# Optimization experiments

Measured on AMD Instinct MI355X. Metric: run time of the kernel, lower is better.

The kernel has to match this reference:

```python
import jax, jax.numpy as jnp
import numpy as np
from jax import lax

N = 100000      # number of nodes (== ninput)
E = 3200000     # number of edges per adjacency
NHID = 128
EPS = 1e-12     # torch F.normalize eps


def spmm(src, dst, w, x):
    # sparse adj @ x : out[i] = sum_{e: dst[e]==i} w[e] * x[src[e]]
    return jax.ops.segment_sum(w[:, None] * x[src], dst, num_segments=N)


def l2norm(x):
    # F.normalize(x, p=2, dim=1)
    n = jnp.sqrt(jnp.sum(x * x, axis=1, keepdims=True))
    return x / jnp.maximum(n, EPS)


def mlp(x, L1, bl1, L2, bl2, L3, bl3):
    # dropout == 0.0 -> identity; chunking is a memory optimization, same math
    h = jax.nn.relu(x @ L1 + bl1)
    h = jax.nn.relu(h @ L2 + bl2)
    return h @ L3 + bl3  # [N, 1]


def setup_inputs() -> dict:
    key = jax.random.key(0)
    ks = jax.random.split(key, 32)
    d = {}
    d["adj1_src"] = jax.random.randint(ks[0], (E,), 0, N, dtype=jnp.int32)
    d["adj1_dst"] = jax.random.randint(ks[1], (E,), 0, N, dtype=jnp.int32)
    d["adj1_w"] = jax.random.uniform(ks[2], (E,), dtype=jnp.float32)
    d["adj2_src"] = jax.random.randint(ks[3], (E,), 0, N, dtype=jnp.int32)
    d["adj2_dst"] = jax.random.randint(ks[4], (E,), 0, N, dtype=jnp.int32)
    d["adj2_w"] = jax.random.uniform(ks[5], (E,), dtype=jnp.float32)
    d["W1"] = jax.random.normal(ks[6], (N, NHID), dtype=jnp.float32) * 0.05
    d["b1"] = jnp.zeros((NHID,), jnp.float32)
    for i, k in zip(range(2, 7), ks[7:12]):
        d[f"W{i}"] = jax.random.normal(k, (NHID, NHID), dtype=jnp.float32) * (1.0 / np.sqrt(NHID))
        d[f"b{i}"] = jnp.zeros((NHID,), jnp.float32)
    d["L1"] = jax.random.normal(ks[12], (NHID, 2 * NHID), dtype=jnp.float32) * (1.0 / np.sqrt(NHID))
    d["bl1"] = jnp.zeros((2 * NHID,), jnp.float32)
    d["L2"] = jax.random.normal(ks[13], (2 * NHID, 2 * NHID), dtype=jnp.float32) * (1.0 / np.sqrt(2 * NHID))
    d["bl2"] = jnp.zeros((2 * NHID,), jnp.float32)
    d["L3"] = jax.random.normal(ks[14], (2 * NHID, 1), dtype=jnp.float32) * (1.0 / np.sqrt(2 * NHID))
    d["bl3"] = jnp.zeros((1,), jnp.float32)
    return d


def reference(adj1_src, adj1_dst, adj1_w, adj2_src, adj2_dst, adj2_w,
              W1, b1, W2, b2, W3, b3, W4, b4, W5, b5, W6, b6,
              L1, bl1, L2, bl2, L3, bl3):
    def branch(src, dst, w):
        x1 = l2norm(jax.nn.relu(spmm(src, dst, w, W1) + b1))
        x2 = l2norm(jax.nn.relu(spmm(src, dst, w, x1 @ W2) + b2))
        x3 = l2norm(jax.nn.relu(spmm(src, dst, w, x2 @ W3) + b3))
        x4 = l2norm(jax.nn.relu(spmm(src, dst, w, x3 @ W4) + b4))
        x5 = l2norm(jax.nn.relu(spmm(src, dst, w, x4 @ W5) + b5))
        x6 = jax.nn.relu(spmm(src, dst, w, x5 @ W6) + b6)
        x7 = lax.stop_gradient(x1 + x2 + x3 + x4 + x5 + x6)  # .detach()
        s = jnp.zeros((N, 1), jnp.float32)
        for xi in (x1, x2, x3, x4, x5):  # computed under torch.no_grad()
            s = s + lax.stop_gradient(mlp(xi, L1, bl1, L2, bl2, L3, bl3))
        s = s + mlp(x6, L1, bl1, L2, bl2, L3, bl3)
        s = s + mlp(x7, L1, bl1, L2, bl2, L3, bl3)
        return s / 7.0

    score1 = branch(adj1_src, adj1_dst, adj1_w)
    score2 = branch(adj2_src, adj2_dst, adj2_w)
    return score1 * score2
```

## Files before the change

### kernel.cpp

```cpp
#include <hip/hip_runtime.h>

#define NN 100000
#define NE 3200000
#define HID 128
#define NNH ((size_t)NN * HID)

typedef __attribute__((ext_vector_type(8))) _Float16 f16x8;
typedef __attribute__((ext_vector_type(4))) _Float16 f16x4;
typedef __attribute__((ext_vector_type(4))) float f32x4;

#define SWZ(row, k) ((k) ^ (((row) & 7) << 3))

__global__ void zero_k(int* p, int n) {
    int i = blockIdx.x * 256 + threadIdx.x;
    if (i < n) p[i] = 0;
}

__global__ void hist_k(const int* __restrict__ dst, int* __restrict__ cnt) {
    int e = blockIdx.x * 256 + threadIdx.x;
    if (e < NE) atomicAdd(&cnt[dst[e]], 1);
}

__global__ __launch_bounds__(1024) void scanA_k(int* __restrict__ rowptr, int* __restrict__ bsum, int n) {
    __shared__ int wsum[16];
    int tid = threadIdx.x;
    int lane = tid & 63, wid = tid >> 6;
    int idx = blockIdx.x * 1024 + tid;
    int v = (idx < n) ? rowptr[idx] : 0;
    int s = v;
#pragma unroll
    for (int o = 1; o < 64; o <<= 1) {
        int t = __shfl_up(s, o, 64);
        if (lane >= o) s += t;
    }
    if (lane == 63) wsum[wid] = s;
    __syncthreads();
    if (wid == 0) {
        int ws = (lane < 16) ? wsum[lane] : 0;
#pragma unroll
        for (int o = 1; o < 16; o <<= 1) {
            int t = __shfl_up(ws, o, 64);
            if (lane >= o) ws += t;
        }
        if (lane < 16) wsum[lane] = ws;
    }
    __syncthreads();
    int woff = (wid == 0) ? 0 : wsum[wid - 1];
    if (idx < n) rowptr[idx] = woff + s - v;
    if (tid == 0) bsum[blockIdx.x] = wsum[15];
}

__global__ void scanB_k(int* __restrict__ bsum, int* __restrict__ rowptr, int nb, int n) {
    if (threadIdx.x == 0) {
        int run = 0;
        for (int i = 0; i < nb; ++i) {
            int t = bsum[i];
            bsum[i] = run;
            run += t;
        }
        rowptr[n] = run;
    }
}

__global__ void scanC_k(int* __restrict__ rowptr, int* __restrict__ cursor,
                        const int* __restrict__ bsum, int n) {
    int idx = blockIdx.x * 256 + threadIdx.x;
    if (idx < n) {
        int v = rowptr[idx] + bsum[idx >> 10];
        rowptr[idx] = v;
        cursor[idx] = v;
    }
}

__global__ void scatter_k(const int* __restrict__ src, const int* __restrict__ dst,
                          const float* __restrict__ w, int* __restrict__ cursor,
                          unsigned* __restrict__ ep) {
    int e = blockIdx.x * 256 + threadIdx.x;
    if (e < NE) {
        int d = dst[e];
        int pos = atomicAdd(&cursor[d], 1);
        ushort hb = __builtin_bit_cast(ushort, (_Float16)w[e]);
        ep[pos] = ((unsigned)src[e] << 15) | (unsigned)hb;
    }
}

template <bool DESC>
__device__ inline unsigned bsort64(unsigned v, int lane) {
#pragma unroll
    for (int k = 2; k <= 64; k <<= 1)
#pragma unroll
        for (int j = k >> 1; j > 0; j >>= 1) {
            unsigned o = __shfl_xor(v, j, 64);
            bool keepmin = ((((lane & j) == 0) == ((lane & k) == 0))) ^ DESC;
            unsigned mn = v < o ? v : o, mx = v < o ? o : v;
            v = keepmin ? mn : mx;
        }
    return v;
}

__device__ inline unsigned bmerge64(unsigned v, int lane) {
#pragma unroll
    for (int j = 32; j > 0; j >>= 1) {
        unsigned o = __shfl_xor(v, j, 64);
        unsigned mn = v < o ? v : o, mx = v < o ? o : v;
        v = ((lane & j) == 0) ? mn : mx;
    }
    return v;
}

__global__ void sort_k(const int* __restrict__ rowptr, unsigned* __restrict__ ep) {
    int row = blockIdx.x * 4 + (threadIdx.x >> 6);
    int lane = threadIdx.x & 63;
    if (row >= NN) return;
    int e0 = rowptr[row], e1 = rowptr[row + 1];
    int deg = e1 - e0;
    if (deg <= 1) return;
    if (deg <= 64) {
        unsigned v = (e0 + lane < e1) ? ep[e0 + lane] : 0xFFFFFFFFu;
        v = bsort64<false>(v, lane);
        if (e0 + lane < e1) ep[e0 + lane] = v;
    } else if (deg <= 128) {
        unsigned a = (e0 + lane < e1) ? ep[e0 + lane] : 0xFFFFFFFFu;
        unsigned b = (e0 + 64 + lane < e1) ? ep[e0 + 64 + lane] : 0xFFFFFFFFu;
        a = bsort64<false>(a, lane);
        b = bsort64<true>(b, lane);
        unsigned mn = a < b ? a : b, mx = a < b ? b : a;
        a = bmerge64(mn, lane);
        b = bmerge64(mx, lane);
        if (e0 + lane < e1) ep[e0 + lane] = a;
        if (e0 + 64 + lane < e1) ep[e0 + 64 + lane] = b;
    }
}

__global__ void convT_k(const float* __restrict__ W, _Float16* __restrict__ WT, int K, int N) {
    int idx = blockIdx.x * 256 + threadIdx.x;
    if (idx < K * N) {
        int k = idx / N, n = idx % N;
        WT[n * K + k] = (_Float16)W[idx];
    }
}

__global__ void conv4_k(const float* __restrict__ A, _Float16* __restrict__ B, int n4) {
    int i = blockIdx.x * 256 + threadIdx.x;
    if (i < n4) {
        float4 v = ((const float4*)A)[i];
        f16x4 h;
        h.x = (_Float16)v.x; h.y = (_Float16)v.y; h.z = (_Float16)v.z; h.w = (_Float16)v.w;
        ((f16x4*)B)[i] = h;
    }
}

template <bool EPI>
__global__ void spmm_k(const _Float16* __restrict__ x, const int* __restrict__ rowptr,
                       const unsigned* __restrict__ ep, const float* __restrict__ bias,
                       _Float16* __restrict__ outx) {
    int row = blockIdx.x * 4 + (threadIdx.x >> 6);
    int l = threadIdx.x & 63;
    int q = l >> 4, li = l & 15;
    if (row >= NN) return;
    int e0 = rowptr[row], e1 = rowptr[row + 1];
    float acc[8] = {};
#pragma unroll 4
    for (int e = e0 + q; e < e1; e += 4) {
        unsigned r = ep[e];
        int s = r >> 15;
        float w = (float)__builtin_bit_cast(_Float16, (ushort)(r & 0x7FFFu));
        f16x8 v = *(const f16x8*)(x + (size_t)s * HID + li * 8);
#pragma unroll
        for (int j = 0; j < 8; ++j) acc[j] += w * (float)v[j];
    }
#pragma unroll
    for (int j = 0; j < 8; ++j) {
        acc[j] += __shfl_xor(acc[j], 16, 64);
        acc[j] += __shfl_xor(acc[j], 32, 64);
    }
    if (EPI) {
        const float4* bp = (const float4*)(bias + li * 8);
        float4 b0 = bp[0], b1 = bp[1];
        acc[0] = fmaxf(acc[0] + b0.x, 0.f); acc[1] = fmaxf(acc[1] + b0.y, 0.f);
        acc[2] = fmaxf(acc[2] + b0.z, 0.f); acc[3] = fmaxf(acc[3] + b0.w, 0.f);
        acc[4] = fmaxf(acc[4] + b1.x, 0.f); acc[5] = fmaxf(acc[5] + b1.y, 0.f);
        acc[6] = fmaxf(acc[6] + b1.z, 0.f); acc[7] = fmaxf(acc[7] + b1.w, 0.f);
        float ss = 0.f;
#pragma unroll
        for (int j = 0; j < 8; ++j) ss += acc[j] * acc[j];
        ss += __shfl_xor(ss, 1, 64);
        ss += __shfl_xor(ss, 2, 64);
        ss += __shfl_xor(ss, 4, 64);
        ss += __shfl_xor(ss, 8, 64);
        float sc = 1.0f / fmaxf(sqrtf(ss), 1e-12f);
#pragma unroll
        for (int j = 0; j < 8; ++j) acc[j] *= sc;
    }
    if (q == 0) {
        f16x8 ho;
#pragma unroll
        for (int j = 0; j < 8; ++j) ho[j] = (_Float16)acc[j];
        *(f16x8*)(outx + (size_t)row * HID + li * 8) = ho;
    }
}

template <bool NORM>
__global__ __launch_bounds__(256) void trans_mlp_k(
    const _Float16* __restrict__ Y,
    const _Float16* __restrict__ WT,
    const float* __restrict__ bw,
    _Float16* __restrict__ Xo,
    const _Float16* __restrict__ L1T, const float* __restrict__ bl1,
    const _Float16* __restrict__ L2T, const float* __restrict__ bl2,
    const float* __restrict__ L3, const float* __restrict__ bl3,
    float* __restrict__ sacc) {
    __shared__ _Float16 Xs[64][128];
    __shared__ _Float16 H1s[64][256];
    __shared__ float red[4][64];
    int t = threadIdx.x;
    int w = t >> 6, l = t & 63;
    int g = l >> 4, li = l & 15;
    int rowBase = blockIdx.x * 64;

#pragma unroll
    for (int i = 0; i < 4; ++i) {
        int idx = t + i * 256;
        int r = idx >> 4, c8 = idx & 15;
        int gr = rowBase + r;
        f16x8 v = (gr < NN) ? *(const f16x8*)(Y + (size_t)gr * 128 + c8 * 8)
                            : (f16x8)(_Float16)0.f;
        *(f16x8*)&Xs[r][SWZ(r, c8 * 8)] = v;
    }
    __syncthreads();

    int cW = w * 32;
    f32x4 accw[4][2] = {};
#pragma unroll
    for (int ks = 0; ks < 4; ++ks) {
        int kb = ks * 32 + g * 8;
        f16x8 a[4];
#pragma unroll
        for (int mt = 0; mt < 4; ++mt) {
            int r = mt * 16 + li;
            a[mt] = *(const f16x8*)&Xs[r][SWZ(r, kb)];
        }
#pragma unroll
        for (int nt = 0; nt < 2; ++nt) {
            f16x8 b = *(const f16x8*)(WT + (size_t)(cW + nt * 16 + li) * 128 + kb);
#pragma unroll
            for (int mt = 0; mt < 4; ++mt)
                accw[mt][nt] = __builtin_amdgcn_mfma_f32_16x16x32_f16(a[mt], b, accw[mt][nt], 0, 0, 0);
        }
    }
    float vv[4][2][4];
    float b0 = bw[cW + li], b1v = bw[cW + 16 + li];
#pragma unroll
    for (int mt = 0; mt < 4; ++mt)
#pragma unroll
        for (int r4 = 0; r4 < 4; ++r4) {
            vv[mt][0][r4] = fmaxf(accw[mt][0][r4] + b0, 0.f);
            vv[mt][1][r4] = fmaxf(accw[mt][1][r4] + b1v, 0.f);
        }
    if (NORM) {
#pragma unroll
        for (int mt = 0; mt < 4; ++mt)
#pragma unroll
            for (int r4 = 0; r4 < 4; ++r4) {
                float ps = vv[mt][0][r4] * vv[mt][0][r4] + vv[mt][1][r4] * vv[mt][1][r4];
                ps += __shfl_xor(ps, 1, 64);
                ps += __shfl_xor(ps, 2, 64);
                ps += __shfl_xor(ps, 4, 64);
                ps += __shfl_xor(ps, 8, 64);
                if (li == 0) red[w][mt * 16 + g * 4 + r4] = ps;
            }
        __syncthreads();
        if (t < 64) {
            float s = red[0][t] + red[1][t] + red[2][t] + red[3][t];
            red[0][t] = 1.f / fmaxf(sqrtf(s), 1e-12f);
        }
        __syncthreads();
    } else {
        __syncthreads();
    }
#pragma unroll
    for (int mt = 0; mt < 4; ++mt)
#pragma unroll
        for (int r4 = 0; r4 < 4; ++r4) {
            int row = mt * 16 + g * 4 + r4;
            float sc = NORM ? red[0][row] : 1.f;
            _Float16 h0 = (_Float16)(vv[mt][0][r4] * sc);
            _Float16 h1 = (_Float16)(vv[mt][1][r4] * sc);
            Xs[row][SWZ(row, cW + li)] = h0;
            Xs[row][SWZ(row, cW + 16 + li)] = h1;
            int gr = rowBase + row;
            if (gr < NN) {
                Xo[(size_t)gr * 128 + cW + li] = h0;
                Xo[(size_t)gr * 128 + cW + 16 + li] = h1;
            }
        }
    __syncthreads();

    int cM = w * 64;
    f32x4 acc[4][4] = {};
#pragma unroll
    for (int ks = 0; ks < 4; ++ks) {
        int kb = ks * 32 + g * 8;
        f16x8 a[4];
#pragma unroll
        for (int mt = 0; mt < 4; ++mt) {
            int r = mt * 16 + li;
            a[mt] = *(const f16x8*)&Xs[r][SWZ(r, kb)];
        }
#pragma unroll
        for (int nt = 0; nt < 4; ++nt) {
            int n = cM + nt * 16 + li;
            f16x8 b = *(const f16x8*)(L1T + (size_t)n * 128 + kb);
#pragma unroll
            for (int mt = 0; mt < 4; ++mt)
                acc[mt][nt] = __builtin_amdgcn_mfma_f32_16x16x32_f16(a[mt], b, acc[mt][nt], 0, 0, 0);
        }
    }
#pragma unroll
    for (int nt = 0; nt < 4; ++nt) {
        int col = cM + nt * 16 + li;
        float bb = bl1[col];
#pragma unroll
        for (int mt = 0; mt < 4; ++mt)
#pragma unroll
            for (int r4 = 0; r4 < 4; ++r4) {
                int row = mt * 16 + g * 4 + r4;
                H1s[row][SWZ(row, col)] = (_Float16)fmaxf(acc[mt][nt][r4] + bb, 0.f);
            }
    }
    __syncthreads();

    f32x4 acc2[4][4] = {};
#pragma unroll
    for (int ks = 0; ks < 8; ++ks) {
        int kb = ks * 32 + g * 8;
        f16x8 a[4];
#pragma unroll
        for (int mt = 0; mt < 4; ++mt) {
            int r = mt * 16 + li;
            a[mt] = *(const f16x8*)&H1s[r][SWZ(r, kb)];
        }
#pragma unroll
        for (int nt = 0; nt < 4; ++nt) {
            int n = cM + nt * 16 + li;
            f16x8 b = *(const f16x8*)(L2T + (size_t)n * 256 + kb);
#pragma unroll
            for (int mt = 0; mt < 4; ++mt)
                acc2[mt][nt] = __builtin_amdgcn_mfma_f32_16x16x32_f16(a[mt], b, acc2[mt][nt], 0, 0, 0);
        }
    }
    float part[4][4] = {};
#pragma unroll
    for (int nt = 0; nt < 4; ++nt) {
        int col = cM + nt * 16 + li;
        float bb = bl2[col];
        float l3v = L3[col];
#pragma unroll
        for (int mt = 0; mt < 4; ++mt)
#pragma unroll
            for (int r4 = 0; r4 < 4; ++r4)
                part[mt][r4] += fmaxf(acc2[mt][nt][r4] + bb, 0.f) * l3v;
    }
#pragma unroll
    for (int mt = 0; mt < 4; ++mt)
#pragma unroll
        for (int r4 = 0; r4 < 4; ++r4) {
            float p = part[mt][r4];
            p += __shfl_xor(p, 1, 64);
            p += __shfl_xor(p, 2, 64);
            p += __shfl_xor(p, 4, 64);
            p += __shfl_xor(p, 8, 64);
            if (li == 0) red[w][mt * 16 + g * 4 + r4] = p;
        }
    __syncthreads();
    if (t < 64) {
        int gr = rowBase + t;
        if (gr < NN)
            sacc[gr] += red[0][t] + red[1][t] + red[2][t] + red[3][t] + bl3[0];
    }
}

template <bool SUM6, bool INIT>
__global__ __launch_bounds__(256) void mlp_fused_k(
    const _Float16* __restrict__ X,
    const _Float16* __restrict__ L1T, const float* __restrict__ bl1,
    const _Float16* __restrict__ L2T, const float* __restrict__ bl2,
    const float* __restrict__ L3, const float* __restrict__ bl3,
    float* __restrict__ sacc) {
    __shared__ _Float16 Xs[64][128];
    __shared__ _Float16 H1s[64][256];
    __shared__ float red[4][64];
    int t = threadIdx.x;
    int w = t >> 6, l = t & 63;
    int g = l >> 4, li = l & 15;
    int rowBase = blockIdx.x * 64;

#pragma unroll
    for (int i = 0; i < 4; ++i) {
        int idx = t + i * 256;
        int r = idx >> 4, c8 = idx & 15;
        int gr = rowBase + r;
        if (SUM6) {
            float s[8] = {};
            if (gr < NN) {
#pragma unroll
                for (int l6 = 0; l6 < 6; ++l6) {
                    f16x8 v = *(const f16x8*)(X + (size_t)l6 * NNH + (size_t)gr * HID + c8 * 8);
#pragma unroll
                    for (int j = 0; j < 8; ++j) s[j] += (float)v[j];
                }
            }
            f16x8 hv;
#pragma unroll
            for (int j = 0; j < 8; ++j) hv[j] = (_Float16)s[j];
            *(f16x8*)&Xs[r][SWZ(r, c8 * 8)] = hv;
        } else {
            f16x8 v = (gr < NN) ? *(const f16x8*)(X + (size_t)gr * HID + c8 * 8)
                                : (f16x8)(_Float16)0.f;
            *(f16x8*)&Xs[r][SWZ(r, c8 * 8)] = v;
        }
    }
    __syncthreads();

    int cM = w * 64;
    f32x4 acc[4][4] = {};
#pragma unroll
    for (int ks = 0; ks < 4; ++ks) {
        int kb = ks * 32 + g * 8;
        f16x8 a[4];
#pragma unroll
        for (int mt = 0; mt < 4; ++mt) {
            int r = mt * 16 + li;
            a[mt] = *(const f16x8*)&Xs[r][SWZ(r, kb)];
        }
#pragma unroll
        for (int nt = 0; nt < 4; ++nt) {
            int n = cM + nt * 16 + li;
            f16x8 b = *(const f16x8*)(L1T + (size_t)n * 128 + kb);
#pragma unroll
            for (int mt = 0; mt < 4; ++mt)
                acc[mt][nt] = __builtin_amdgcn_mfma_f32_16x16x32_f16(a[mt], b, acc[mt][nt], 0, 0, 0);
        }
    }
#pragma unroll
    for (int nt = 0; nt < 4; ++nt) {
        int col = cM + nt * 16 + li;
        float bb = bl1[col];
#pragma unroll
        for (int mt = 0; mt < 4; ++mt)
#pragma unroll
            for (int r4 = 0; r4 < 4; ++r4) {
                int row = mt * 16 + g * 4 + r4;
                H1s[row][SWZ(row, col)] = (_Float16)fmaxf(acc[mt][nt][r4] + bb, 0.f);
            }
    }
    __syncthreads();

    f32x4 acc2[4][4] = {};
#pragma unroll
    for (int ks = 0; ks < 8; ++ks) {
        int kb = ks * 32 + g * 8;
        f16x8 a[4];
#pragma unroll
        for (int mt = 0; mt < 4; ++mt) {
            int r = mt * 16 + li;
            a[mt] = *(const f16x8*)&H1s[r][SWZ(r, kb)];
        }
#pragma unroll
        for (int nt = 0; nt < 4; ++nt) {
            int n = cM + nt * 16 + li;
            f16x8 b = *(const f16x8*)(L2T + (size_t)n * 256 + kb);
#pragma unroll
            for (int mt = 0; mt < 4; ++mt)
                acc2[mt][nt] = __builtin_amdgcn_mfma_f32_16x16x32_f16(a[mt], b, acc2[mt][nt], 0, 0, 0);
        }
    }
    float part[4][4] = {};
#pragma unroll
    for (int nt = 0; nt < 4; ++nt) {
        int col = cM + nt * 16 + li;
        float bb = bl2[col];
        float l3v = L3[col];
#pragma unroll
        for (int mt = 0; mt < 4; ++mt)
#pragma unroll
            for (int r4 = 0; r4 < 4; ++r4)
                part[mt][r4] += fmaxf(acc2[mt][nt][r4] + bb, 0.f) * l3v;
    }
#pragma unroll
    for (int mt = 0; mt < 4; ++mt)
#pragma unroll
        for (int r4 = 0; r4 < 4; ++r4) {
            float p = part[mt][r4];
            p += __shfl_xor(p, 1, 64);
            p += __shfl_xor(p, 2, 64);
            p += __shfl_xor(p, 4, 64);
            p += __shfl_xor(p, 8, 64);
            if (li == 0) red[w][mt * 16 + g * 4 + r4] = p;
        }
    __syncthreads();
    if (t < 64) {
        int gr = rowBase + t;
        if (gr < NN) {
            float s = red[0][t] + red[1][t] + red[2][t] + red[3][t] + bl3[0];
            if (INIT) sacc[gr] = s; else sacc[gr] += s;
        }
    }
}

__global__ void score_store_k(const float* __restrict__ sacc, float* __restrict__ dst) {
    int i = blockIdx.x * 256 + threadIdx.x;
    if (i < NN) dst[i] = sacc[i] * (1.f / 7.f);
}

__global__ void final_mul_k(const float* __restrict__ sacc, const float* __restrict__ score1,
                            float* __restrict__ out) {
    int i = blockIdx.x * 256 + threadIdx.x;
    if (i < NN) out[i] = score1[i] * (sacc[i] * (1.f / 7.f));
}

extern "C" void kernel_launch(void* const* d_in, const int* in_sizes, int n_in,
                              void* d_out, int out_size, void* d_ws, size_t ws_size,
                              hipStream_t stream) {
    const int* asrc[2] = {(const int*)d_in[0], (const int*)d_in[3]};
    const int* adst[2] = {(const int*)d_in[1], (const int*)d_in[4]};
    const float* aw[2] = {(const float*)d_in[2], (const float*)d_in[5]};
    const float* W1 = (const float*)d_in[6];
    const float* b1 = (const float*)d_in[7];
    const float* Wk[5] = {(const float*)d_in[8], (const float*)d_in[10], (const float*)d_in[12],
                          (const float*)d_in[14], (const float*)d_in[16]};
    const float* bk[5] = {(const float*)d_in[9], (const float*)d_in[11], (const float*)d_in[13],
                          (const float*)d_in[15], (const float*)d_in[17]};
    const float* L1 = (const float*)d_in[18];
    const float* bl1 = (const float*)d_in[19];
    const float* L2 = (const float*)d_in[20];
    const float* bl2 = (const float*)d_in[21];
    const float* L3 = (const float*)d_in[22];
    const float* bl3 = (const float*)d_in[23];
    float* out = (float*)d_out;

    char* p = (char*)d_ws;
    _Float16* L1T = (_Float16*)p; p += 65536;
    _Float16* L2T = (_Float16*)p; p += 131072;
    _Float16* WkT = (_Float16*)p; p += 163840;
    _Float16* W1h = (_Float16*)p; p += NNH * 2;
    _Float16* tmp = (_Float16*)p; p += NNH * 2;
    _Float16* xbuf = (_Float16*)p; p += 6 * NNH * 2;
    float* sacc = (float*)p; p += (size_t)NN * 4;
    float* score1 = (float*)p; p += (size_t)NN * 4;
    unsigned* ep = (unsigned*)p; p += (size_t)NE * 4;
    int* rowptr = (int*)p; p += (size_t)(NN + 1) * 4;
    int* cursor = (int*)p; p += (size_t)NN * 4;
    int* bsum = (int*)p; p += 512;

    const int GE = (NE + 255) / 256;
    const int GN = (NN + 255) / 256;
    const int GS = (NN + 3) / 4;
    const int GM = (NN + 63) / 64;
    const int NB = (NN + 1023) / 1024;

    convT_k<<<(128 * 256 + 255) / 256, 256, 0, stream>>>(L1, L1T, 128, 256);
    convT_k<<<(256 * 256 + 255) / 256, 256, 0, stream>>>(L2, L2T, 256, 256);
    for (int l = 0; l < 5; ++l)
        convT_k<<<(128 * 128 + 255) / 256, 256, 0, stream>>>(Wk[l], WkT + (size_t)l * 16384, 128, 128);
    conv4_k<<<(NN * HID / 4 + 255) / 256, 256, 0, stream>>>(W1, W1h, NN * HID / 4);

    for (int br = 0; br < 2; ++br) {
        zero_k<<<GN, 256, 0, stream>>>(rowptr, NN + 1);
        hist_k<<<GE, 256, 0, stream>>>(adst[br], rowptr);
        scanA_k<<<NB, 1024, 0, stream>>>(rowptr, bsum, NN);
        scanB_k<<<1, 64, 0, stream>>>(bsum, rowptr, NB, NN);
        scanC_k<<<GN, 256, 0, stream>>>(rowptr, cursor, bsum, NN);
        scatter_k<<<GE, 256, 0, stream>>>(asrc[br], adst[br], aw[br], cursor, ep);
        sort_k<<<GS, 256, 0, stream>>>(rowptr, ep);

        spmm_k<true><<<GS, 256, 0, stream>>>(W1h, rowptr, ep, b1, xbuf);
        mlp_fused_k<false, true><<<GM, 256, 0, stream>>>(xbuf, L1T, bl1, L2T, bl2, L3, bl3, sacc);

        for (int l = 0; l < 5; ++l) {
            spmm_k<false><<<GS, 256, 0, stream>>>(xbuf + (size_t)l * NNH, rowptr, ep, b1, tmp);
            _Float16* xo = xbuf + (size_t)(l + 1) * NNH;
            if (l < 4)
                trans_mlp_k<true><<<GM, 256, 0, stream>>>(tmp, WkT + (size_t)l * 16384, bk[l], xo,
                                                          L1T, bl1, L2T, bl2, L3, bl3, sacc);
            else
                trans_mlp_k<false><<<GM, 256, 0, stream>>>(tmp, WkT + (size_t)l * 16384, bk[l], xo,
                                                           L1T, bl1, L2T, bl2, L3, bl3, sacc);
        }

        mlp_fused_k<true, false><<<GM, 256, 0, stream>>>(xbuf, L1T, bl1, L2T, bl2, L3, bl3, sacc);

        if (br == 0)
            score_store_k<<<GN, 256, 0, stream>>>(sacc, score1);
        else
            final_mul_k<<<GN, 256, 0, stream>>>(sacc, score1, out);
    }
}
```

Measured before the change: 2.842 ms.

## Window SpMM by source-row ranges to improve gather cache locality

Adds a bounds kernel that binary-searches each row's sorted edge list to split it into 8 source-node windows. The SpMM is rewritten so each block owns 33 destination rows in each of two halves and sweeps windows in order, accumulating partial sums in shared memory. All blocks then read the same source-row range at about the same time, which should keep the gathered feature rows cache-resident. The costs are extra per-window bound loads, one wave handling each row-window serially with 2 halves per lane, fewer blocks in flight, and no guarantee that blocks stay in step.

```diff
diff --git a/kernel.cpp b/kernel.cpp
--- a/kernel.cpp
+++ b/kernel.cpp
@@ -4,9 +4,15 @@
 #define NE 3200000
 #define HID 128
 #define NNH ((size_t)NN * HID)
+#define HALF 50000
+#define NWIN 8
+#define WROWS 12500
+#define RPB 33
+#define NBLK 1516
 
 typedef __attribute__((ext_vector_type(8))) _Float16 f16x8;
 typedef __attribute__((ext_vector_type(4))) _Float16 f16x4;
+typedef __attribute__((ext_vector_type(2))) _Float16 f16x2;
 typedef __attribute__((ext_vector_type(4))) float f32x4;
 
 #define SWZ(row, k) ((k) ^ (((row) & 7) << 3))
@@ -132,6 +138,24 @@
     }
 }
 
+__global__ void bounds_k(const int* __restrict__ rowptr, const unsigned* __restrict__ ep,
+                         int* __restrict__ bnd) {
+    int r = blockIdx.x * 256 + threadIdx.x;
+    if (r >= NN) return;
+    int e0 = rowptr[r], e1 = rowptr[r + 1];
+    bnd[r] = e0;
+    bnd[(size_t)NWIN * NN + r] = e1;
+    for (int wdx = 1; wdx < NWIN; ++wdx) {
+        unsigned key = (unsigned)(wdx * WROWS) << 15;
+        int lo = e0, hi = e1;
+        while (lo < hi) {
+            int mid = (lo + hi) >> 1;
+            if (ep[mid] < key) lo = mid + 1; else hi = mid;
+        }
+        bnd[(size_t)wdx * NN + r] = lo;
+    }
+}
+
 __global__ void convT_k(const float* __restrict__ W, _Float16* __restrict__ WT, int K, int N) {
     int idx = blockIdx.x * 256 + threadIdx.x;
     if (idx < K * N) {
@@ -151,61 +175,67 @@
 }
 
 template <bool EPI>
-__global__ void spmm_k(const _Float16* __restrict__ x, const int* __restrict__ rowptr,
-                       const unsigned* __restrict__ ep, const float* __restrict__ bias,
-                       _Float16* __restrict__ outx) {
-    int row = blockIdx.x * 4 + (threadIdx.x >> 6);
-    int l = threadIdx.x & 63;
-    int q = l >> 4, li = l & 15;
-    if (row >= NN) return;
-    int e0 = rowptr[row], e1 = rowptr[row + 1];
-    float acc[8] = {};
+__global__ __launch_bounds__(256) void spmm_win_k(const _Float16* __restrict__ x,
+                                                  const int* __restrict__ bnd,
+                                                  const unsigned* __restrict__ ep,
+                                                  const float* __restrict__ bias,
+                                                  _Float16* __restrict__ outx) {
+    __shared__ float accs[RPB][HID];
+    int tid = threadIdx.x;
+    int w = tid >> 6, lane = tid & 63;
+    for (int g = 0; g < 2; ++g) {
+        int rowBase = g * HALF + blockIdx.x * RPB;
+        int rowLim = (g + 1) * HALF;
+        for (int i = tid; i < RPB * HID; i += 256) ((float*)accs)[i] = 0.f;
+        __syncthreads();
+        for (int win = 0; win < NWIN; ++win) {
+            const int* b0p = bnd + (size_t)win * NN;
+            const int* b1p = bnd + (size_t)(win + 1) * NN;
+            for (int j = w; j < RPB; j += 4) {
+                int r = rowBase + j;
+                if (r >= rowLim) break;
+                int e0 = b0p[r], e1 = b1p[r];
+                if (e0 == e1) continue;
+                float a0 = 0.f, a1 = 0.f;
 #pragma unroll 4
-    for (int e = e0 + q; e < e1; e += 4) {
-        unsigned r = ep[e];
-        int s = r >> 15;
-        float w = (float)__builtin_bit_cast(_Float16, (ushort)(r & 0x7FFFu));
-        f16x8 v = *(const f16x8*)(x + (size_t)s * HID + li * 8);
-#pragma unroll
-        for (int j = 0; j < 8; ++j) acc[j] += w * (float)v[j];
-    }
-#pragma unroll
-    for (int j = 0; j < 8; ++j) {
-        acc[j] += __shfl_xor(acc[j], 16, 64);
-        acc[j] += __shfl_xor(acc[j], 32, 64);
-    }
-    if (EPI) {
-        const float4* bp = (const float4*)(bias + li * 8);
-        float4 b0 = bp[0], b1 = bp[1];
-        acc[0] = fmaxf(acc[0] + b0.x, 0.f); acc[1] = fmaxf(acc[1] + b0.y, 0.f);
-        acc[2] = fmaxf(acc[2] + b0.z, 0.f); acc[3] = fmaxf(acc[3] + b0.w, 0.f);
-        acc[4] = fmaxf(acc[4] + b1.x, 0.f); acc[5] = fmaxf(acc[5] + b1.y, 0.f);
-        acc[6] = fmaxf(acc[6] + b1.z, 0.f); acc[7] = fmaxf(acc[7] + b1.w, 0.f);
-        float ss = 0.f;
-#pragma unroll
-        for (int j = 0; j < 8; ++j) ss += acc[j] * acc[j];
-        ss += __shfl_xor(ss, 1, 64);
-        ss += __shfl_xor(ss, 2, 64);
-        ss += __shfl_xor(ss, 4, 64);
-        ss += __shfl_xor(ss, 8, 64);
-        float sc = 1.0f / fmaxf(sqrtf(ss), 1e-12f);
-#pragma unroll
-        for (int j = 0; j < 8; ++j) acc[j] *= sc;
-    }
-    if (q == 0) {
-        f16x8 ho;
-#pragma unroll
-        for (int j = 0; j < 8; ++j) ho[j] = (_Float16)acc[j];
-        *(f16x8*)(outx + (size_t)row * HID + li * 8) = ho;
+                for (int e = e0; e < e1; ++e) {
+                    unsigned rec = ep[e];
+                    float wgt = (float)__builtin_bit_cast(_Float16, (ushort)(rec & 0x7FFFu));
+                    unsigned s = rec >> 15;
+                    f16x2 v = *(const f16x2*)(x + (size_t)s * HID + lane * 2);
+                    a0 += wgt * (float)v.x;
+                    a1 += wgt * (float)v.y;
+                }
+                accs[j][lane * 2] += a0;
+                accs[j][lane * 2 + 1] += a1;
+            }
+        }
+        __syncthreads();
+        for (int j = w; j < RPB; j += 4) {
+            int r = rowBase + j;
+            if (r >= rowLim) break;
+            float a0 = accs[j][lane * 2], a1 = accs[j][lane * 2 + 1];
+            if (EPI) {
+                a0 = fmaxf(a0 + bias[lane * 2], 0.f);
+                a1 = fmaxf(a1 + bias[lane * 2 + 1], 0.f);
+                float ss = a0 * a0 + a1 * a1;
+#pragma unroll
+                for (int o = 32; o >= 1; o >>= 1) ss += __shfl_xor(ss, o, 64);
+                float sc = 1.0f / fmaxf(sqrtf(ss), 1e-12f);
+                a0 *= sc; a1 *= sc;
+            }
+            f16x2 ho;
+            ho.x = (_Float16)a0; ho.y = (_Float16)a1;
+            *(f16x2*)(outx + (size_t)r * HID + lane * 2) = ho;
+        }
+        __syncthreads();
     }
 }
 
 template <bool NORM>
 __global__ __launch_bounds__(256) void trans_mlp_k(
-    const _Float16* __restrict__ Y,
-    const _Float16* __restrict__ WT,
-    const float* __restrict__ bw,
-    _Float16* __restrict__ Xo,
+    const _Float16* __restrict__ Y, const _Float16* __restrict__ WT,
+    const float* __restrict__ bw, _Float16* __restrict__ Xo,
     const _Float16* __restrict__ L1T, const float* __restrict__ bl1,
     const _Float16* __restrict__ L2T, const float* __restrict__ bl2,
     const float* __restrict__ L3, const float* __restrict__ bl3,
@@ -552,6 +582,7 @@
     int* rowptr = (int*)p; p += (size_t)(NN + 1) * 4;
     int* cursor = (int*)p; p += (size_t)NN * 4;
     int* bsum = (int*)p; p += 512;
+    int* bnd = (int*)p; p += (size_t)(NWIN + 1) * NN * 4;
 
     const int GE = (NE + 255) / 256;
     const int GN = (NN + 255) / 256;
@@ -573,12 +604,13 @@
         scanC_k<<<GN, 256, 0, stream>>>(rowptr, cursor, bsum, NN);
         scatter_k<<<GE, 256, 0, stream>>>(asrc[br], adst[br], aw[br], cursor, ep);
         sort_k<<<GS, 256, 0, stream>>>(rowptr, ep);
-
-        spmm_k<true><<<GS, 256, 0, stream>>>(W1h, rowptr, ep, b1, xbuf);
+        bounds_k<<<GN, 256, 0, stream>>>(rowptr, ep, bnd);
+
+        spmm_win_k<true><<<NBLK, 256, 0, stream>>>(W1h, bnd, ep, b1, xbuf);
         mlp_fused_k<false, true><<<GM, 256, 0, stream>>>(xbuf, L1T, bl1, L2T, bl2, L3, bl3, sacc);
 
         for (int l = 0; l < 5; ++l) {
-            spmm_k<false><<<GS, 256, 0, stream>>>(xbuf + (size_t)l * NNH, rowptr, ep, b1, tmp);
+            spmm_win_k<false><<<NBLK, 256, 0, stream>>>(xbuf + (size_t)l * NNH, bnd, ep, b1, tmp);
             _Float16* xo = xbuf + (size_t)(l + 1) * NNH;
             if (l < 4)
                 trans_mlp_k<true><<<GM, 256, 0, stream>>>(tmp, WkT + (size_t)l * 16384, bk[l], xo,
```

Measured after the change: 4.826 ms. 1.7x slower.
